# Kernel optimization log

Hardware: AMD Instinct MI355X
Metric: run time of the kernel (lower is better)

Reference implementation:

```python
import jax, jax.numpy as jnp
import numpy as np

B, NB, DIM = 4096, 64, 256
CNT_R = 500
CNT_E = CNT_R * 2  # padding relation id == CNT_E maps to the masked row
N_WR = CNT_R * 2 + 1
N_ZQ = CNT_R * 2


def setup_inputs() -> dict:
    key = jax.random.key(0)
    ks = jax.random.split(key, 10)
    batch_nei_rid = jax.random.randint(ks[0], (B, NB), 0, N_WR, dtype=jnp.int64 if jax.config.read('jax_enable_x64') else jnp.int32)
    batch_nei_e_emb = jax.random.normal(ks[1], (B, NB, DIM), dtype=jnp.float32)
    batch_nei_rw = jax.random.uniform(ks[2], (B, NB), dtype=jnp.float32)
    batch_q_rid = jax.random.randint(ks[3], (B,), 0, N_ZQ, dtype=jnp.int32)
    # xavier-normal-ish params
    def xav(k, shape):
        fan_in, fan_out = shape[-1], shape[-2] if len(shape) > 1 else shape[-1]
        std = (2.0 / (fan_in + fan_out)) ** 0.5
        return (jax.random.normal(k, shape) * std).astype(jnp.float32)
    w_r_weight = xav(ks[4], (N_WR, DIM))
    zq_weight = xav(ks[5], (N_ZQ, DIM))
    attn_W_w = xav(ks[6], (2 * DIM, 2 * DIM))   # [out, in], torch Linear layout
    attn_W_b = jnp.zeros((2 * DIM,), jnp.float32)
    u_a_w = xav(ks[7], (1, 2 * DIM))
    u_a_b = jnp.zeros((1,), jnp.float32)
    return {
        'batch_nei_rid': batch_nei_rid,
        'batch_nei_e_emb': batch_nei_e_emb,
        'batch_nei_rw': batch_nei_rw,
        'batch_q_rid': batch_q_rid,
        'w_r_weight': w_r_weight,
        'zq_weight': zq_weight,
        'attn_W_w': attn_W_w,
        'attn_W_b': attn_W_b,
        'u_a_w': u_a_w,
        'u_a_b': u_a_b,
    }


def reference(batch_nei_rid, batch_nei_e_emb, batch_nei_rw, batch_q_rid,
              w_r_weight, zq_weight, attn_W_w, attn_W_b, u_a_w, u_a_b):
    # relation hyperplane gather + TransH-style projection
    w_r = w_r_weight[batch_nei_rid]                                   # [B,NB,D]
    nrm = jnp.maximum(jnp.linalg.norm(w_r, axis=-1, keepdims=True), 1e-12)
    wn = w_r / nrm                                                    # f.normalize(p=2)
    e_tr = batch_nei_e_emb - jnp.sum(batch_nei_e_emb * wn, axis=-1, keepdims=True) * wn
    # mask_emb: 1 for real rows, 0 for padding row (index CNT_E)
    mask = (batch_nei_rid < CNT_E).astype(e_tr.dtype)[..., None]
    e_tr = e_tr * mask
    # nn attention: concat(z_q, e_Tr) -> Linear -> tanh -> Linear(1)
    z_q = zq_weight[batch_q_rid][:, None, :]                          # [B,1,D]
    cat = jnp.concatenate([jnp.broadcast_to(z_q, e_tr.shape), e_tr], axis=-1)  # [B,NB,2D]
    h = jnp.tanh(jnp.einsum('bni,oi->bno', cat, attn_W_w) + attn_W_b)
    _alpha = jnp.einsum('bni,oi->bno', h, u_a_w)[..., 0] + u_a_b[0]   # [B,NB]
    # mask_weight: 1e19 at padding row, subtracted before softmax
    _alpha = _alpha - jnp.where(batch_nei_rid == CNT_E, jnp.asarray(1e19, _alpha.dtype), jnp.asarray(0.0, _alpha.dtype))
    alpha = jax.nn.softmax(_alpha, axis=-1)
    attn = alpha + batch_nei_rw                                       # use_logic_attention
    return jnp.sum(attn[..., None] * e_tr, axis=-2)                   # [B,D]
```

## Files before the change

kernel.cpp:

```cpp
#include <hip/hip_runtime.h>
#include <math.h>

#define NB    64
#define DIM   256
#define TWOD  512
#define CNTE  1000
#define E2S   264

typedef __attribute__((ext_vector_type(8))) short short8;
typedef __attribute__((ext_vector_type(4))) float f32x4;

union U16x8 { uint4 u; short8 s; };

__device__ __forceinline__ unsigned short f2bf(float x) {
    unsigned int u = __float_as_uint(x);
    u += 0x7fffu + ((u >> 16) & 1u);
    return (unsigned short)(u >> 16);
}
__device__ __forceinline__ float bf2f(unsigned short h) {
    return __uint_as_float(((unsigned int)h) << 16);
}
__device__ __forceinline__ float tanh_fast(float x) {
    float e = __expf(2.0f * x);
    return 1.0f - 2.0f / (e + 1.0f);
}

__global__ __launch_bounds__(256) void pack_w_kernel(
    const float* __restrict__ attn_W, unsigned short* __restrict__ wbf)
{
    int f = blockIdx.x * 256 + threadIdx.x;
    int j    = f & 7;
    int lane = (f >> 3) & 63;
    int kt   = (f >> 9) & 15;
    int ot   = f >> 13;
    int o = ot * 16 + (lane & 15);
    int k = kt * 32 + (lane >> 4) * 8 + j;
    wbf[f] = f2bf(attn_W[(size_t)o * TWOD + k]);
}

__global__ __launch_bounds__(256, 2) void encoder_attn_kernel(
    const int*   __restrict__ nei_rid,
    const float* __restrict__ nei_e,
    const float* __restrict__ nei_rw,
    const int*   __restrict__ q_rid,
    const float* __restrict__ w_r,
    const float* __restrict__ zq_w,
    const float* __restrict__ attn_b,
    const float* __restrict__ u_a_w,
    const float* __restrict__ u_a_b,
    const unsigned short* __restrict__ wbf,
    float*       __restrict__ out)
{
    __shared__ __align__(16) unsigned short e2[NB * E2S];
    __shared__ __align__(16) unsigned short zq2[DIM];
    __shared__ float2 bua[TWOD];
    __shared__ float  red_a[256];
    __shared__ float  pen[NB];
    __shared__ float  attn_lds[NB];

    const int b = blockIdx.x;
    const int t = threadIdx.x;

    const int qr = q_rid[b];
    bua[t]       = make_float2(attn_b[t],       u_a_w[t]);
    bua[t + 256] = make_float2(attn_b[t + 256], u_a_w[t + 256]);
    zq2[t] = f2bf(zq_w[(size_t)qr * DIM + t]);

    const int n = t >> 2, q = t & 3;
    const int rid = nei_rid[b * NB + n];
    const float4* e4 = (const float4*)(nei_e + ((size_t)(b * NB + n)) * DIM) + q * 16;
    const float4* w4 = (const float4*)(w_r + (size_t)rid * DIM) + q * 16;
    {
        float4 ev[16], wv[16];
        float sew = 0.f, sww = 0.f;
        #pragma unroll
        for (int j = 0; j < 16; ++j) {
            ev[j] = e4[j]; wv[j] = w4[j];
            sew += ev[j].x * wv[j].x + ev[j].y * wv[j].y + ev[j].z * wv[j].z + ev[j].w * wv[j].w;
            sww += wv[j].x * wv[j].x + wv[j].y * wv[j].y + wv[j].z * wv[j].z + wv[j].w * wv[j].w;
        }
        sew += __shfl_xor(sew, 1); sew += __shfl_xor(sew, 2);
        sww += __shfl_xor(sww, 1); sww += __shfl_xor(sww, 2);
        float nc   = fmaxf(sqrtf(sww), 1e-12f);
        float coef = sew / (nc * nc);
        float maskf = (rid < CNTE) ? 1.f : 0.f;
        if (q == 0) pen[n] = (rid == CNTE) ? 1e19f : 0.f;
        unsigned short* e2row = e2 + n * E2S + q * 64;
        #pragma unroll
        for (int jj = 0; jj < 8; ++jj) {
            float4 e0 = ev[jj * 2],     w0 = wv[jj * 2];
            float4 e1 = ev[jj * 2 + 1], w1 = wv[jj * 2 + 1];
            uint4 pk;
            pk.x = (unsigned int)f2bf((e0.x - coef * w0.x) * maskf)
                 | ((unsigned int)f2bf((e0.y - coef * w0.y) * maskf) << 16);
            pk.y = (unsigned int)f2bf((e0.z - coef * w0.z) * maskf)
                 | ((unsigned int)f2bf((e0.w - coef * w0.w) * maskf) << 16);
            pk.z = (unsigned int)f2bf((e1.x - coef * w1.x) * maskf)
                 | ((unsigned int)f2bf((e1.y - coef * w1.y) * maskf) << 16);
            pk.w = (unsigned int)f2bf((e1.z - coef * w1.z) * maskf)
                 | ((unsigned int)f2bf((e1.w - coef * w1.w) * maskf) << 16);
            *(uint4*)(e2row + jj * 8) = pk;
        }
    }
    __syncthreads();

    const int wv_id = t >> 6;
    const int lane  = t & 63;
    const int l15 = lane & 15, lq = lane >> 4;

    short8 afrag[4][8];
    #pragma unroll
    for (int mt = 0; mt < 4; ++mt)
        #pragma unroll
        for (int kt = 0; kt < 8; ++kt) {
            const unsigned short* p = e2 + (mt * 16 + l15) * E2S + kt * 32 + lq * 8;
            U16x8 u; u.u = *(const uint4*)p;
            afrag[mt][kt] = u.s;
        }

    f32x4 lpv[4];
    #pragma unroll
    for (int mt = 0; mt < 4; ++mt) lpv[mt] = (f32x4){0.f, 0.f, 0.f, 0.f};

    #pragma unroll 1
    for (int ot = 0; ot < 8; ++ot) {
        const int otg = wv_id * 8 + ot;
        const uint4* wp = (const uint4*)wbf + (size_t)(otg * 16) * 64 + lane;
        short8 bz[8], be[8];
        #pragma unroll
        for (int kt = 0; kt < 8; ++kt) { U16x8 u; u.u = wp[kt * 64]; bz[kt] = u.s; }
        #pragma unroll
        for (int kt = 0; kt < 8; ++kt) { U16x8 u; u.u = wp[(kt + 8) * 64]; be[kt] = u.s; }

        f32x4 accz = (f32x4){0.f, 0.f, 0.f, 0.f};
        #pragma unroll
        for (int kt = 0; kt < 8; ++kt) {
            U16x8 u; u.u = *(const uint4*)(zq2 + kt * 32 + lq * 8);
            accz = __builtin_amdgcn_mfma_f32_16x16x32_bf16(u.s, bz[kt], accz, 0, 0, 0);
        }
        f32x4 acc[4];
        #pragma unroll
        for (int mt = 0; mt < 4; ++mt) acc[mt] = accz;
        #pragma unroll
        for (int kt = 0; kt < 8; ++kt)
            #pragma unroll
            for (int mt = 0; mt < 4; ++mt)
                acc[mt] = __builtin_amdgcn_mfma_f32_16x16x32_bf16(
                              afrag[mt][kt], be[kt], acc[mt], 0, 0, 0);

        float2 zu = bua[otg * 16 + l15];
        #pragma unroll
        for (int mt = 0; mt < 4; ++mt)
            #pragma unroll
            for (int r = 0; r < 4; ++r) {
                float h = tanh_fast(acc[mt][r] + zu.x);
                lpv[mt][r] += zu.y * h;
            }
    }

    #pragma unroll
    for (int mt = 0; mt < 4; ++mt)
        #pragma unroll
        for (int r = 0; r < 4; ++r) {
            float v = lpv[mt][r];
            v += __shfl_xor(v, 1); v += __shfl_xor(v, 2);
            v += __shfl_xor(v, 4); v += __shfl_xor(v, 8);
            if (l15 == 0) red_a[wv_id * 64 + mt * 16 + lq * 4 + r] = v;
        }
    __syncthreads();

    if (t < NB) {
        float lgt = red_a[t] + red_a[64 + t] + red_a[128 + t] + red_a[192 + t]
                  + u_a_b[0] - pen[t];
        float m = lgt;
        #pragma unroll
        for (int off = 32; off > 0; off >>= 1) m = fmaxf(m, __shfl_xor(m, off));
        float ex = __expf(lgt - m);
        float s = ex;
        #pragma unroll
        for (int off = 32; off > 0; off >>= 1) s += __shfl_xor(s, off);
        attn_lds[t] = ex / s + nei_rw[b * NB + t];
    }
    __syncthreads();

    float oacc = 0.f;
    #pragma unroll 8
    for (int nn = 0; nn < NB; ++nn)
        oacc += attn_lds[nn] * bf2f(e2[nn * E2S + t]);
    out[(size_t)b * DIM + t] = oacc;
}

extern "C" void kernel_launch(void* const* d_in, const int* in_sizes, int n_in,
                              void* d_out, int out_size, void* d_ws, size_t ws_size,
                              hipStream_t stream) {
    const int*   nei_rid = (const int*)  d_in[0];
    const float* nei_e   = (const float*)d_in[1];
    const float* nei_rw  = (const float*)d_in[2];
    const int*   q_rid   = (const int*)  d_in[3];
    const float* w_r     = (const float*)d_in[4];
    const float* zq_w    = (const float*)d_in[5];
    const float* attn_W  = (const float*)d_in[6];
    const float* attn_b  = (const float*)d_in[7];
    const float* u_a_w   = (const float*)d_in[8];
    const float* u_a_b   = (const float*)d_in[9];
    float* out = (float*)d_out;

    const int B = in_sizes[3];

    unsigned short* wbf = (unsigned short*)d_ws;

    hipLaunchKernelGGL(pack_w_kernel, dim3(1024), dim3(256), 0, stream, attn_W, wbf);
    hipLaunchKernelGGL(encoder_attn_kernel, dim3(B), dim3(256), 0, stream,
                       nei_rid, nei_e, nei_rw, q_rid, w_r, zq_w,
                       attn_b, u_a_w, u_a_b, wbf, out);
}
```

Before: 525.4 us.

## Store projected embeddings in MFMA fragment layout and stream A-fragments from LDS

The projected neighbor embeddings are now written to shared memory directly in the MFMA A-fragment order, with the padded row stride dropped. The kernel no longer holds all 32 A-fragments in registers; each k-step reloads four fragments from LDS, and launch bounds rise from 2 to 3 blocks per SIMD. The final weighted sum is rewritten over the fragment layout with shuffle reductions and vectorized stores. This trades more LDS reads inside the inner loop for lower register pressure and higher occupancy.

```diff
diff --git a/kernel.cpp b/kernel.cpp
--- a/kernel.cpp
+++ b/kernel.cpp
@@ -5,7 +5,6 @@
 #define DIM   256
 #define TWOD  512
 #define CNTE  1000
-#define E2S   264
 
 typedef __attribute__((ext_vector_type(8))) short short8;
 typedef __attribute__((ext_vector_type(4))) float f32x4;
@@ -38,7 +37,7 @@
     wbf[f] = f2bf(attn_W[(size_t)o * TWOD + k]);
 }
 
-__global__ __launch_bounds__(256, 2) void encoder_attn_kernel(
+__global__ __launch_bounds__(256, 3) void encoder_attn_kernel(
     const int*   __restrict__ nei_rid,
     const float* __restrict__ nei_e,
     const float* __restrict__ nei_rw,
@@ -51,7 +50,7 @@
     const unsigned short* __restrict__ wbf,
     float*       __restrict__ out)
 {
-    __shared__ __align__(16) unsigned short e2[NB * E2S];
+    __shared__ __align__(16) unsigned short e2[NB * DIM];
     __shared__ __align__(16) unsigned short zq2[DIM];
     __shared__ float2 bua[TWOD];
     __shared__ float  red_a[256];
@@ -85,7 +84,7 @@
         float coef = sew / (nc * nc);
         float maskf = (rid < CNTE) ? 1.f : 0.f;
         if (q == 0) pen[n] = (rid == CNTE) ? 1e19f : 0.f;
-        unsigned short* e2row = e2 + n * E2S + q * 64;
+        const int mt1 = n >> 4, l15n = n & 15;
         #pragma unroll
         for (int jj = 0; jj < 8; ++jj) {
             float4 e0 = ev[jj * 2],     w0 = wv[jj * 2];
@@ -99,7 +98,10 @@
                  | ((unsigned int)f2bf((e1.y - coef * w1.y) * maskf) << 16);
             pk.w = (unsigned int)f2bf((e1.z - coef * w1.z) * maskf)
                  | ((unsigned int)f2bf((e1.w - coef * w1.w) * maskf) << 16);
-            *(uint4*)(e2row + jj * 8) = pk;
+            int kt = 2 * q + (jj >> 2);
+            int lq = jj & 3;
+            int off = (((mt1 * 8 + kt) * 64) + lq * 16 + l15n) * 8;
+            *(uint4*)(e2 + off) = pk;
         }
     }
     __syncthreads();
@@ -107,16 +109,6 @@
     const int wv_id = t >> 6;
     const int lane  = t & 63;
     const int l15 = lane & 15, lq = lane >> 4;
-
-    short8 afrag[4][8];
-    #pragma unroll
-    for (int mt = 0; mt < 4; ++mt)
-        #pragma unroll
-        for (int kt = 0; kt < 8; ++kt) {
-            const unsigned short* p = e2 + (mt * 16 + l15) * E2S + kt * 32 + lq * 8;
-            U16x8 u; u.u = *(const uint4*)p;
-            afrag[mt][kt] = u.s;
-        }
 
     f32x4 lpv[4];
     #pragma unroll
@@ -142,12 +134,17 @@
         #pragma unroll
         for (int mt = 0; mt < 4; ++mt) acc[mt] = accz;
         #pragma unroll
-        for (int kt = 0; kt < 8; ++kt)
-            #pragma unroll
-            for (int mt = 0; mt < 4; ++mt)
-                acc[mt] = __builtin_amdgcn_mfma_f32_16x16x32_bf16(
-                              afrag[mt][kt], be[kt], acc[mt], 0, 0, 0);
-
+        for (int kt = 0; kt < 8; ++kt) {
+            short8 a0, a1, a2, a3;
+            { U16x8 u; u.u = *(const uint4*)(e2 + ((0 * 8 + kt) * 64 + lane) * 8); a0 = u.s; }
+            { U16x8 u; u.u = *(const uint4*)(e2 + ((1 * 8 + kt) * 64 + lane) * 8); a1 = u.s; }
+            { U16x8 u; u.u = *(const uint4*)(e2 + ((2 * 8 + kt) * 64 + lane) * 8); a2 = u.s; }
+            { U16x8 u; u.u = *(const uint4*)(e2 + ((3 * 8 + kt) * 64 + lane) * 8); a3 = u.s; }
+            acc[0] = __builtin_amdgcn_mfma_f32_16x16x32_bf16(a0, be[kt], acc[0], 0, 0, 0);
+            acc[1] = __builtin_amdgcn_mfma_f32_16x16x32_bf16(a1, be[kt], acc[1], 0, 0, 0);
+            acc[2] = __builtin_amdgcn_mfma_f32_16x16x32_bf16(a2, be[kt], acc[2], 0, 0, 0);
+            acc[3] = __builtin_amdgcn_mfma_f32_16x16x32_bf16(a3, be[kt], acc[3], 0, 0, 0);
+        }
         float2 zu = bua[otg * 16 + l15];
         #pragma unroll
         for (int mt = 0; mt < 4; ++mt)
@@ -183,11 +180,33 @@
     }
     __syncthreads();
 
-    float oacc = 0.f;
-    #pragma unroll 8
-    for (int nn = 0; nn < NB; ++nn)
-        oacc += attn_lds[nn] * bf2f(e2[nn * E2S + t]);
-    out[(size_t)b * DIM + t] = oacc;
+    #pragma unroll
+    for (int ktl = 0; ktl < 2; ++ktl) {
+        const int kt = wv_id * 2 + ktl;
+        float vacc[8];
+        #pragma unroll
+        for (int j = 0; j < 8; ++j) vacc[j] = 0.f;
+        #pragma unroll
+        for (int mt = 0; mt < 4; ++mt) {
+            U16x8 u; u.u = *(const uint4*)(e2 + ((mt * 8 + kt) * 64 + lane) * 8);
+            float an = attn_lds[mt * 16 + l15];
+            #pragma unroll
+            for (int j = 0; j < 8; ++j)
+                vacc[j] += an * bf2f((unsigned short)u.s[j]);
+        }
+        #pragma unroll
+        for (int j = 0; j < 8; ++j) {
+            vacc[j] += __shfl_xor(vacc[j], 1);
+            vacc[j] += __shfl_xor(vacc[j], 2);
+            vacc[j] += __shfl_xor(vacc[j], 4);
+            vacc[j] += __shfl_xor(vacc[j], 8);
+        }
+        if (l15 == 0) {
+            float* op = out + (size_t)b * DIM + kt * 32 + lq * 8;
+            ((float4*)op)[0] = make_float4(vacc[0], vacc[1], vacc[2], vacc[3]);
+            ((float4*)op)[1] = make_float4(vacc[4], vacc[5], vacc[6], vacc[7]);
+        }
+    }
 }
 
 extern "C" void kernel_launch(void* const* d_in, const int* in_sizes, int n_in,
```

Measured after the change: 774.7 us. 1.47x slower.
